# Kernel tuning notes

Measured on AMD Instinct MI355X. Metric: run time of the kernel, lower is better.

Reference implementation:

```python
import jax, jax.numpy as jnp
import numpy as np

EPS = 1e-8  # EPSILON in original repo (sharpen denom); cosine eps matches torch default 1e-8
MAX_SHIFT = 1
M_FEAT = 128


def _lstm_cell(x, h, c, W_ih, W_hh, b_ih, b_hh):
    gates = x @ W_ih.T + b_ih + h @ W_hh.T + b_hh
    i, f, g, o = jnp.split(gates, 4, axis=1)
    c_new = jax.nn.sigmoid(f) * c + jax.nn.sigmoid(i) * jnp.tanh(g)
    h_new = jax.nn.sigmoid(o) * jnp.tanh(c_new)
    return h_new, c_new


def _content_address(bank, k, b):
    # torch cosine_similarity over dim 2: dot / max(|m||k|, eps)
    dot = jnp.einsum('bnm,bm->bn', bank, k)
    denom = jnp.maximum(jnp.linalg.norm(bank, axis=2) * jnp.linalg.norm(k, axis=1, keepdims=True), 1e-8)
    return jax.nn.softmax(b * dot / denom, axis=1)


def _shift(w, s):
    # circular unroll then valid cross-correlation with per-batch kernel s [B, 2*MAX_SHIFT+1]
    wp = jnp.concatenate([w[:, -MAX_SHIFT:], w, w[:, :MAX_SHIFT]], axis=1)
    N = w.shape[1]
    taps = 2 * MAX_SHIFT + 1
    return sum(s[:, i:i + 1] * wp[:, i:i + N] for i in range(taps))


def _sharpen(w, r):
    wr = w ** r
    return wr / (wr.sum(axis=1, keepdims=True) + EPS)


def _move(bank, w_prev, k, b, g, s, r):
    w = _content_address(bank, k, b)
    w = w + (1.0 - g) * w_prev  # faithful: w_c is NOT scaled by g in the source
    w = _shift(w, s)
    return _sharpen(w, r)


def _split_read(p):
    M = M_FEAT
    k = p[:, :M]
    b = jax.nn.softplus(p[:, M:M + 1])
    g = jax.nn.sigmoid(p[:, M + 1:M + 2])
    s = jax.nn.softmax(p[:, M + 2:M + 5], axis=1)
    r = 1.0 + jax.nn.softplus(p[:, M + 5:M + 6])
    return k, b, g, s, r


def _split_write(p):
    M = M_FEAT
    k, b, g, s, r = _split_read(p[:, :M + 6])
    e = jax.nn.sigmoid(p[:, M + 6:M + 6 + M])
    a = p[:, M + 6 + M:M + 6 + 2 * M]
    return k, b, g, s, r, e, a


def setup_inputs() -> dict:
    key = jax.random.key(0)
    ks = jax.random.split(key, 16)
    B, E, H, N, M, O = 64, 256, 512, 4096, 128, 256
    rd_out, wr_out = M + 2 * MAX_SHIFT + 4, 3 * M + 2 * MAX_SHIFT + 4
    sc = 0.05
    return {
        'x': jax.random.normal(ks[0], (B, E), jnp.float32),
        'h_prev': jax.random.normal(ks[1], (B, H), jnp.float32),
        'c_prev': jax.random.normal(ks[2], (B, H), jnp.float32),
        'bank': jax.random.normal(ks[3], (B, N, M), jnp.float32) * 0.1,
        'read_w_prev': jnp.zeros((3, B, N), jnp.float32),
        'write_w_prev': jnp.zeros((3, B, N), jnp.float32),
        'W_ih': jax.random.normal(ks[4], (4 * H, E), jnp.float32) * sc,
        'W_hh': jax.random.normal(ks[5], (4 * H, H), jnp.float32) * sc,
        'b_ih': jax.random.normal(ks[6], (4 * H,), jnp.float32) * sc,
        'b_hh': jax.random.normal(ks[7], (4 * H,), jnp.float32) * sc,
        'read_W': jax.random.normal(ks[8], (3, rd_out, H), jnp.float32) * sc,
        'read_b': jax.random.normal(ks[9], (3, rd_out), jnp.float32) * sc,
        'write_W': jax.random.normal(ks[10], (3, wr_out, H), jnp.float32) * sc,
        'write_b': jax.random.normal(ks[11], (3, wr_out), jnp.float32) * sc,
        'out_W': jax.random.normal(ks[12], (O, 3 * M + H), jnp.float32) * sc,
        'out_b': jax.random.normal(ks[13], (O,), jnp.float32) * sc,
    }


def reference(x, h_prev, c_prev, bank, read_w_prev, write_w_prev,
              W_ih, W_hh, b_ih, b_hh, read_W, read_b, write_W, write_b,
              out_W, out_b):
    h, c = _lstm_cell(x, h_prev, c_prev, W_ih, W_hh, b_ih, b_hh)
    reads = []
    for i in range(3):  # head_num=3, structurally distinct params per head
        # write head: update bank
        pw = h @ write_W[i].T + write_b[i]
        k, b, g, s, r, e, a = _split_write(pw)
        ww = _move(bank, write_w_prev[i], k, b, g, s, r)
        bank = bank * (1.0 - ww[:, :, None] * e[:, None, :]) + ww[:, :, None] * a[:, None, :]
        # read head: read from updated bank
        pr = h @ read_W[i].T + read_b[i]
        k, b, g, s, r = _split_read(pr)
        wr = _move(bank, read_w_prev[i], k, b, g, s, r)
        reads.append(jnp.einsum('bn,bnm->bm', wr, bank))
    out = jnp.concatenate(reads + [h], axis=1) @ out_W.T + out_b
    return out
```

## Files before the change

kernel.cpp:

```cpp
#include <hip/hip_runtime.h>
#include <math.h>

namespace {

constexpr int kB = 64;
constexpr int kN = 4096;
constexpr int kM = 128;
constexpr int kH = 512;
constexpr int kE = 256;
constexpr int kO = 256;
constexpr int kGates = 4 * kH;
constexpr int kCatW = 3 * kM + kH;
constexpr int kPRow = 1600;
constexpr int kWN = kB * kN;

__device__ __forceinline__ float sigm_(float x) { return 1.f / (1.f + expf(-x)); }
__device__ __forceinline__ float softplus_(float x) { return x > 20.f ? x : log1pf(expf(x)); }

__global__ __launch_bounds__(256) void init_ws_k(float* gates, float* praw, float* cat,
                                                 float* out, const float* __restrict__ out_b) {
  int idx = blockIdx.x * 256 + threadIdx.x;
  if (idx < kB * kGates) gates[idx] = 0.f;
  if (idx < kB * kPRow)  praw[idx] = 0.f;
  if (idx < kB * 3 * kM) cat[(idx / 384) * kCatW + (idx % 384)] = 0.f;
  if (idx < kB * kO)     out[idx] = out_b[idx & (kO - 1)];
}

__global__ __launch_bounds__(256) void gemm_tn(const float* __restrict__ A, int lda,
                                               const float* __restrict__ W, int ldw,
                                               float* __restrict__ C, int ldc, int c0, int J) {
  __shared__ float As[64][68];
  __shared__ float Ws[64][68];
  const int tid = threadIdx.x;
  const int j0 = blockIdx.x * 64;
  const int b0 = (tid & 15) * 4;
  const int j4 = (tid >> 4) * 4;
  float acc[4][4] = {};
  for (int kc = 0; kc < 2; kc++) {
    const int k0 = blockIdx.y * 128 + kc * 64;
    __syncthreads();
#pragma unroll
    for (int i = 0; i < 4; i++) {
      int idx = tid + i * 256;
      int bb = idx >> 4;
      int kk = (idx & 15) * 4;
      float4 v = *(const float4*)(A + (size_t)bb * lda + k0 + kk);
      As[kk][bb] = v.x; As[kk + 1][bb] = v.y; As[kk + 2][bb] = v.z; As[kk + 3][bb] = v.w;
      float4 w = make_float4(0.f, 0.f, 0.f, 0.f);
      if (j0 + bb < J) w = *(const float4*)(W + (size_t)(j0 + bb) * ldw + k0 + kk);
      Ws[kk][bb] = w.x; Ws[kk + 1][bb] = w.y; Ws[kk + 2][bb] = w.z; Ws[kk + 3][bb] = w.w;
    }
    __syncthreads();
#pragma unroll 2
    for (int k = 0; k < 64; k++) {
      float4 av = *(const float4*)&As[k][b0];
      float4 wv = *(const float4*)&Ws[k][j4];
      float aa[4] = {av.x, av.y, av.z, av.w};
      float wwv[4] = {wv.x, wv.y, wv.z, wv.w};
#pragma unroll
      for (int ii = 0; ii < 4; ii++)
#pragma unroll
        for (int jj = 0; jj < 4; jj++) acc[ii][jj] += aa[ii] * wwv[jj];
    }
  }
#pragma unroll
  for (int ii = 0; ii < 4; ii++)
#pragma unroll
    for (int jj = 0; jj < 4; jj++) {
      int j = j0 + j4 + jj;
      if (j < J) atomicAdd(&C[(size_t)(b0 + ii) * ldc + c0 + j], acc[ii][jj]);
    }
}

__global__ __launch_bounds__(256) void lstm_nl(const float* __restrict__ gates,
                                               const float* __restrict__ b_ih,
                                               const float* __restrict__ b_hh,
                                               const float* __restrict__ c_prev,
                                               float* __restrict__ cat) {
  int idx = blockIdx.x * 256 + threadIdx.x;
  if (idx >= kB * kH) return;
  int b = idx >> 9;
  int hh = idx & (kH - 1);
  const float* g = gates + (size_t)b * kGates;
  float i_ = g[hh]            + b_ih[hh]            + b_hh[hh];
  float f_ = g[kH + hh]       + b_ih[kH + hh]       + b_hh[kH + hh];
  float g_ = g[2 * kH + hh]   + b_ih[2 * kH + hh]   + b_hh[2 * kH + hh];
  float o_ = g[3 * kH + hh]   + b_ih[3 * kH + hh]   + b_hh[3 * kH + hh];
  float c = sigm_(f_) * c_prev[idx] + sigm_(i_) * tanhf(g_);
  float h = sigm_(o_) * tanhf(c);
  cat[(size_t)b * kCatW + 3 * kM + hh] = h;
}

__global__ __launch_bounds__(128) void split_params(const float* __restrict__ praw,
                                                    const float* __restrict__ write_b,
                                                    const float* __restrict__ read_b,
                                                    float* __restrict__ kwb, float* __restrict__ krb,
                                                    float* __restrict__ evb, float* __restrict__ avb,
                                                    float* __restrict__ scal) {
  const int b = blockIdx.x;
  const int m = threadIdx.x;
  __shared__ float red[2];
  for (int i = 0; i < 3; i++) {
    const float* p = praw + (size_t)b * kPRow + i * 390;
    const float* wb = write_b + i * 390;
    float kv = p[m] + wb[m];
    kwb[((size_t)i * kB + b) * kM + m] = kv;
    evb[((size_t)i * kB + b) * kM + m] = sigm_(p[134 + m] + wb[134 + m]);
    avb[((size_t)i * kB + b) * kM + m] = p[262 + m] + wb[262 + m];
    float sq = kv * kv;
#pragma unroll
    for (int mm = 1; mm < 64; mm <<= 1) sq += __shfl_xor(sq, mm, 64);
    __syncthreads();
    if ((m & 63) == 0) red[m >> 6] = sq;
    __syncthreads();
    if (m == 0) {
      float* s = scal + ((size_t)i * kB + b) * 8;
      s[0] = softplus_(p[128] + wb[128]);
      s[1] = sigm_(p[129] + wb[129]);
      s[2] = 1.f + softplus_(p[133] + wb[133]);
      float x0 = p[130] + wb[130], x1 = p[131] + wb[131], x2 = p[132] + wb[132];
      float mx = fmaxf(x0, fmaxf(x1, x2));
      float e0 = expf(x0 - mx), e1 = expf(x1 - mx), e2 = expf(x2 - mx);
      float si = 1.f / (e0 + e1 + e2);
      s[3] = e0 * si; s[4] = e1 * si; s[5] = e2 * si;
      s[6] = sqrtf(red[0] + red[1]);
    }
  }
  for (int i = 0; i < 3; i++) {
    const float* p = praw + (size_t)b * kPRow + 1170 + i * 134;
    const float* rb = read_b + i * 134;
    float kv = p[m] + rb[m];
    krb[((size_t)i * kB + b) * kM + m] = kv;
    float sq = kv * kv;
#pragma unroll
    for (int mm = 1; mm < 64; mm <<= 1) sq += __shfl_xor(sq, mm, 64);
    __syncthreads();
    if ((m & 63) == 0) red[m >> 6] = sq;
    __syncthreads();
    if (m == 0) {
      float* s = scal + ((size_t)(3 + i) * kB + b) * 8;
      s[0] = softplus_(p[128] + rb[128]);
      s[1] = sigm_(p[129] + rb[129]);
      s[2] = 1.f + softplus_(p[133] + rb[133]);
      float x0 = p[130] + rb[130], x1 = p[131] + rb[131], x2 = p[132] + rb[132];
      float mx = fmaxf(x0, fmaxf(x1, x2));
      float e0 = expf(x0 - mx), e1 = expf(x1 - mx), e2 = expf(x2 - mx);
      float si = 1.f / (e0 + e1 + e2);
      s[3] = e0 * si; s[4] = e1 * si; s[5] = e2 * si;
      s[6] = sqrtf(red[0] + red[1]);
    }
  }
}

struct BankArgs {
  const float* bank;
  const float* cw[3];
  const float* ev[3];
  const float* av[3];
  const float* rw[3];
  float* ro[3];
  const float* k1;
  const float* k2;
  float* s1; float* s2; float* ssq;
};

template <int NC>
__global__ __launch_bounds__(256) void bank_pass(BankArgs A) {
  const int b = blockIdx.y;
  const int tid = threadIdx.x;
  const int lane = tid & 63;
  const int wv = tid >> 6;
  const int sub = lane >> 4;
  const int lm = lane & 15;
  const int m8 = lm * 8;
  constexpr int NCA = (NC > 0) ? NC : 1;
  float e_r[NCA][8], a_r[NCA][8];
#pragma unroll
  for (int j = 0; j < NC; j++)
#pragma unroll
    for (int t = 0; t < 8; t++) {
      e_r[j][t] = A.ev[j][b * kM + m8 + t];
      a_r[j][t] = A.av[j][b * kM + m8 + t];
    }
  const bool has1 = (A.s1 != nullptr);
  const bool has2 = (A.s2 != nullptr);
  float k1r[8] = {}, k2r[8] = {};
  if (has1) {
#pragma unroll
    for (int t = 0; t < 8; t++) k1r[t] = A.k1[b * kM + m8 + t];
  }
  if (has2) {
#pragma unroll
    for (int t = 0; t < 8; t++) k2r[t] = A.k2[b * kM + m8 + t];
  }
  float racc[3][8];
#pragma unroll
  for (int j = 0; j < 3; j++)
#pragma unroll
    for (int t = 0; t < 8; t++) racc[j][t] = 0.f;
  __shared__ float rlds[3][kM];
  if (tid < kM) { rlds[0][tid] = 0.f; rlds[1][tid] = 0.f; rlds[2][tid] = 0.f; }

  const size_t bbase = (size_t)b * kN * kM;
  const size_t brow = (size_t)b * kN;
  for (int it = 0; it < 16; it++) {
    const int row = blockIdx.x * 256 + it * 16 + wv * 4 + sub;
    const float* rp = A.bank + bbase + (size_t)row * kM + m8;
    float4 u0 = *(const float4*)rp;
    float4 u1 = *(const float4*)(rp + 4);
    float v[8] = {u0.x, u0.y, u0.z, u0.w, u1.x, u1.y, u1.z, u1.w};
#pragma unroll
    for (int j = 0; j < NC; j++) {
      const float wj = A.cw[j][brow + row];
#pragma unroll
      for (int t = 0; t < 8; t++) v[t] += wj * (a_r[j][t] - e_r[j][t] * v[t]);
      if (A.rw[j]) {
        const float rv = A.rw[j][brow + row];
#pragma unroll
        for (int t = 0; t < 8; t++) racc[j][t] += rv * v[t];
      }
    }
    if (has1) {
      float d1 = 0.f, d2 = 0.f, sq = 0.f;
#pragma unroll
      for (int t = 0; t < 8; t++) { d1 += v[t] * k1r[t]; sq += v[t] * v[t]; }
      if (has2) {
#pragma unroll
        for (int t = 0; t < 8; t++) d2 += v[t] * k2r[t];
      }
#pragma unroll
      for (int m = 1; m < 16; m <<= 1) {
        d1 += __shfl_xor(d1, m, 64);
        sq += __shfl_xor(sq, m, 64);
        if (has2) d2 += __shfl_xor(d2, m, 64);
      }
      if (lm == 0) {
        A.s1[brow + row] = d1;
        A.ssq[brow + row] = sq;
        if (has2) A.s2[brow + row] = d2;
      }
    }
  }
  if (A.rw[0] || A.rw[1] || A.rw[2]) {
    __syncthreads();
#pragma unroll
    for (int j = 0; j < 3; j++) {
      if (!A.rw[j]) continue;
#pragma unroll
      for (int t = 0; t < 8; t++) {
        racc[j][t] += __shfl_xor(racc[j][t], 16, 64);
        racc[j][t] += __shfl_xor(racc[j][t], 32, 64);
      }
      if (sub == 0) {
#pragma unroll
        for (int t = 0; t < 8; t++) atomicAdd(&rlds[j][m8 + t], racc[j][t]);
      }
    }
    __syncthreads();
    if (tid < kM) {
#pragma unroll
      for (int j = 0; j < 3; j++)
        if (A.rw[j]) atomicAdd(&A.ro[j][(size_t)b * kCatW + tid], rlds[j][tid]);
    }
  }
}

struct AddrArgs {
  const float* S[2];
  const float* R[2];
  const float* scal[2];
  const float* wprev[2];
  float* wout[2];
};

__global__ __launch_bounds__(256) void addressing(AddrArgs A) {
  const int b = blockIdx.x;
  const int hs = blockIdx.y;
  const float* S = A.S[hs] + (size_t)b * kN;
  const float* R = A.R[hs] + (size_t)b * kN;
  const float* sc = A.scal[hs] + b * 8;
  const float* wp = A.wprev[hs] + (size_t)b * kN;
  float* wo = A.wout[hs] + (size_t)b * kN;
  const float beta = sc[0], g = sc[1], r = sc[2];
  const float s0 = sc[3], s1 = sc[4], s2 = sc[5], kn = sc[6];
  __shared__ float wb[kN];
  __shared__ float red[4];
  const int tid = threadIdx.x;
  const int lane = tid & 63, wid = tid >> 6;
  float loc[16];
  float mx = -1e30f;
#pragma unroll
  for (int i = 0; i < 16; i++) {
    int n = tid + i * 256;
    float denom = fmaxf(sqrtf(R[n]) * kn, 1e-8f);
    float v = beta * S[n] / denom;
    loc[i] = v;
    mx = fmaxf(mx, v);
  }
#pragma unroll
  for (int m = 1; m < 64; m <<= 1) mx = fmaxf(mx, __shfl_xor(mx, m, 64));
  if (lane == 0) red[wid] = mx;
  __syncthreads();
  mx = fmaxf(fmaxf(red[0], red[1]), fmaxf(red[2], red[3]));
  float sum = 0.f;
#pragma unroll
  for (int i = 0; i < 16; i++) { loc[i] = expf(loc[i] - mx); sum += loc[i]; }
#pragma unroll
  for (int m = 1; m < 64; m <<= 1) sum += __shfl_xor(sum, m, 64);
  __syncthreads();
  if (lane == 0) red[wid] = sum;
  __syncthreads();
  sum = red[0] + red[1] + red[2] + red[3];
  const float inv = 1.f / sum;
  const float omg = 1.f - g;
#pragma unroll
  for (int i = 0; i < 16; i++) {
    int n = tid + i * 256;
    wb[n] = loc[i] * inv + omg * wp[n];
  }
  __syncthreads();
  float ssum = 0.f;
#pragma unroll
  for (int i = 0; i < 16; i++) {
    int n = tid + i * 256;
    float sh = s0 * wb[(n + kN - 1) & (kN - 1)] + s1 * wb[n] + s2 * wb[(n + 1) & (kN - 1)];
    float y = powf(sh, r);
    loc[i] = y;
    ssum += y;
  }
#pragma unroll
  for (int m = 1; m < 64; m <<= 1) ssum += __shfl_xor(ssum, m, 64);
  __syncthreads();
  if (lane == 0) red[wid] = ssum;
  __syncthreads();
  ssum = red[0] + red[1] + red[2] + red[3];
  const float invs = 1.f / (ssum + 1e-8f);
#pragma unroll
  for (int i = 0; i < 16; i++) {
    int n = tid + i * 256;
    wo[n] = loc[i] * invs;
  }
}

}

extern "C" void kernel_launch(void* const* d_in, const int* in_sizes, int n_in,
                              void* d_out, int out_size, void* d_ws, size_t ws_size,
                              hipStream_t stream) {
  const float* x            = (const float*)d_in[0];
  const float* h_prev       = (const float*)d_in[1];
  const float* c_prev       = (const float*)d_in[2];
  const float* bank         = (const float*)d_in[3];
  const float* read_w_prev  = (const float*)d_in[4];
  const float* write_w_prev = (const float*)d_in[5];
  const float* W_ih         = (const float*)d_in[6];
  const float* W_hh         = (const float*)d_in[7];
  const float* b_ih         = (const float*)d_in[8];
  const float* b_hh         = (const float*)d_in[9];
  const float* read_W       = (const float*)d_in[10];
  const float* read_b       = (const float*)d_in[11];
  const float* write_W      = (const float*)d_in[12];
  const float* write_b      = (const float*)d_in[13];
  const float* out_W        = (const float*)d_in[14];
  const float* out_b        = (const float*)d_in[15];
  float* out = (float*)d_out;

  float* ws    = (float*)d_ws;
  float* gates = ws;
  float* praw  = gates + kB * kGates;
  float* cat   = praw + kB * kPRow;
  float* kwb   = cat + kB * kCatW;
  float* krb   = kwb + 3 * kB * kM;
  float* evb   = krb + 3 * kB * kM;
  float* avb   = evb + 3 * kB * kM;
  float* scal  = avb + 3 * kB * kM;
  float* S1    = scal + 6 * kB * 8;
  float* S2    = S1 + kWN;
  float* SSq   = S2 + kWN;
  float* wwv   = SSq + kWN;
  float* wrv   = wwv + 3 * kWN;

  init_ws_k<<<512, 256, 0, stream>>>(gates, praw, cat, out, out_b);
  gemm_tn<<<dim3(kGates / 64, kE / 128), 256, 0, stream>>>(x, kE, W_ih, kE, gates, kGates, 0, kGates);
  gemm_tn<<<dim3(kGates / 64, kH / 128), 256, 0, stream>>>(h_prev, kH, W_hh, kH, gates, kGates, 0, kGates);
  lstm_nl<<<(kB * kH) / 256, 256, 0, stream>>>(gates, b_ih, b_hh, c_prev, cat);
  gemm_tn<<<dim3(19, kH / 128), 256, 0, stream>>>(cat + 3 * kM, kCatW, write_W, kH, praw, kPRow, 0, 1170);
  gemm_tn<<<dim3(7, kH / 128), 256, 0, stream>>>(cat + 3 * kM, kCatW, read_W, kH, praw, kPRow, 1170, 402);
  split_params<<<64, 128, 0, stream>>>(praw, write_b, read_b, kwb, krb, evb, avb, scal);

  {
    BankArgs p = {};
    p.bank = bank;
    p.k1 = kwb; p.s1 = S1; p.s2 = nullptr; p.ssq = SSq;
    bank_pass<0><<<dim3(16, kB), 256, 0, stream>>>(p);
  }
  {
    AddrArgs a = {};
    a.S[0] = S1; a.R[0] = SSq; a.scal[0] = scal + 0;
    a.wprev[0] = write_w_prev; a.wout[0] = wwv;
    a.S[1] = a.S[0]; a.R[1] = a.R[0]; a.scal[1] = a.scal[0]; a.wprev[1] = a.wprev[0]; a.wout[1] = a.wout[0];
    addressing<<<dim3(64, 1), 256, 0, stream>>>(a);
  }
  {
    BankArgs p = {};
    p.bank = bank;
    p.cw[0] = wwv; p.ev[0] = evb; p.av[0] = avb;
    p.k1 = krb; p.k2 = kwb + kB * kM;
    p.s1 = S1; p.s2 = S2; p.ssq = SSq;
    bank_pass<1><<<dim3(16, kB), 256, 0, stream>>>(p);
  }
  {
    AddrArgs a = {};
    a.S[0] = S1; a.R[0] = SSq; a.scal[0] = scal + (size_t)3 * kB * 8;
    a.wprev[0] = read_w_prev; a.wout[0] = wrv;
    a.S[1] = S2; a.R[1] = SSq; a.scal[1] = scal + (size_t)1 * kB * 8;
    a.wprev[1] = write_w_prev + kWN; a.wout[1] = wwv + kWN;
    addressing<<<dim3(64, 2), 256, 0, stream>>>(a);
  }
  {
    BankArgs p = {};
    p.bank = bank;
    p.cw[0] = wwv;        p.ev[0] = evb;            p.av[0] = avb;
    p.cw[1] = wwv + kWN;  p.ev[1] = evb + kB * kM;  p.av[1] = avb + kB * kM;
    p.rw[0] = wrv; p.ro[0] = cat;
    p.k1 = krb + kB * kM; p.k2 = kwb + 2 * kB * kM;
    p.s1 = S1; p.s2 = S2; p.ssq = SSq;
    bank_pass<2><<<dim3(16, kB), 256, 0, stream>>>(p);
  }
  {
    AddrArgs a = {};
    a.S[0] = S1; a.R[0] = SSq; a.scal[0] = scal + (size_t)4 * kB * 8;
    a.wprev[0] = read_w_prev + kWN; a.wout[0] = wrv + kWN;
    a.S[1] = S2; a.R[1] = SSq; a.scal[1] = scal + (size_t)2 * kB * 8;
    a.wprev[1] = write_w_prev + 2 * kWN; a.wout[1] = wwv + 2 * kWN;
    addressing<<<dim3(64, 2), 256, 0, stream>>>(a);
  }
  {
    BankArgs p = {};
    p.bank = bank;
    p.cw[0] = wwv;           p.ev[0] = evb;                p.av[0] = avb;
    p.cw[1] = wwv + kWN;     p.ev[1] = evb + kB * kM;      p.av[1] = avb + kB * kM;
    p.cw[2] = wwv + 2 * kWN; p.ev[2] = evb + 2 * kB * kM;  p.av[2] = avb + 2 * kB * kM;
    p.k1 = krb + 2 * kB * kM;
    p.s1 = S1; p.s2 = nullptr; p.ssq = SSq;
    bank_pass<3><<<dim3(16, kB), 256, 0, stream>>>(p);
  }
  {
    AddrArgs a = {};
    a.S[0] = S1; a.R[0] = SSq; a.scal[0] = scal + (size_t)5 * kB * 8;
    a.wprev[0] = read_w_prev + 2 * kWN; a.wout[0] = wrv + 2 * kWN;
    a.S[1] = a.S[0]; a.R[1] = a.R[0]; a.scal[1] = a.scal[0]; a.wprev[1] = a.wprev[0]; a.wout[1] = a.wout[0];
    addressing<<<dim3(64, 1), 256, 0, stream>>>(a);
  }
  {
    BankArgs p = {};
    p.bank = bank;
    p.cw[0] = wwv;           p.ev[0] = evb;                p.av[0] = avb;
    p.cw[1] = wwv + kWN;     p.ev[1] = evb + kB * kM;      p.av[1] = avb + kB * kM;
    p.cw[2] = wwv + 2 * kWN; p.ev[2] = evb + 2 * kB * kM;  p.av[2] = avb + 2 * kB * kM;
    p.rw[1] = wrv + kWN;     p.ro[1] = cat + kM;
    p.rw[2] = wrv + 2 * kWN; p.ro[2] = cat + 2 * kM;
    p.s1 = nullptr; p.s2 = nullptr; p.ssq = nullptr;
    bank_pass<3><<<dim3(16, kB), 256, 0, stream>>>(p);
  }
  gemm_tn<<<dim3(kO / 64, kCatW / 128), 256, 0, stream>>>(cat, kCatW, out_W, kCatW, out, kO, 0, kO);

  (void)in_sizes; (void)n_in; (void)out_size; (void)ws_size;
}
```

Baseline: 494.0 us.

## Fuse addressing into bank passes via last-block counters and merge GEMM launches

The separate addressing kernels are folded into the tail of each bank_pass. An atomic per-batch counter lets the last of the 16 blocks for a batch compute the softmax, shift and sharpen weights. The small GEMMs are merged: the x and h gate GEMMs become one non-split-K kernel that writes directly and also does the workspace init, and the write and read projections become one kernel. This removes launches, atomics and zero-init passes. The cost is that the gate and projection GEMMs now run on very few blocks (33 and 25) with the full K loop each, and each pass now uses distinct scratch buffers.

```diff
diff --git a/kernel.cpp b/kernel.cpp
--- a/kernel.cpp
+++ b/kernel.cpp
@@ -17,18 +17,22 @@
 __device__ __forceinline__ float sigm_(float x) { return 1.f / (1.f + expf(-x)); }
 __device__ __forceinline__ float softplus_(float x) { return x > 20.f ? x : log1pf(expf(x)); }
 
-__global__ __launch_bounds__(256) void init_ws_k(float* gates, float* praw, float* cat,
-                                                 float* out, const float* __restrict__ out_b) {
-  int idx = blockIdx.x * 256 + threadIdx.x;
-  if (idx < kB * kGates) gates[idx] = 0.f;
-  if (idx < kB * kPRow)  praw[idx] = 0.f;
-  if (idx < kB * 3 * kM) cat[(idx / 384) * kCatW + (idx % 384)] = 0.f;
-  if (idx < kB * kO)     out[idx] = out_b[idx & (kO - 1)];
-}
-
-__global__ __launch_bounds__(256) void gemm_tn(const float* __restrict__ A, int lda,
-                                               const float* __restrict__ W, int ldw,
-                                               float* __restrict__ C, int ldc, int c0, int J) {
+__global__ __launch_bounds__(256) void gates_gemm(const float* __restrict__ x,
+                                                  const float* __restrict__ W_ih,
+                                                  const float* __restrict__ h_prev,
+                                                  const float* __restrict__ W_hh,
+                                                  float* __restrict__ gates,
+                                                  const float* __restrict__ out_b,
+                                                  float* __restrict__ out,
+                                                  float* __restrict__ cat,
+                                                  int* __restrict__ cnt) {
+  if (blockIdx.x == 32) {
+    const int tid = threadIdx.x;
+    for (int i = tid; i < kB * kO; i += 256) out[i] = out_b[i & (kO - 1)];
+    for (int i = tid; i < kB * 384; i += 256) cat[(i / 384) * kCatW + (i % 384)] = 0.f;
+    for (int i = tid; i < 512; i += 256) cnt[i] = 0;
+    return;
+  }
   __shared__ float As[64][68];
   __shared__ float Ws[64][68];
   const int tid = threadIdx.x;
@@ -36,8 +40,12 @@
   const int b0 = (tid & 15) * 4;
   const int j4 = (tid >> 4) * 4;
   float acc[4][4] = {};
-  for (int kc = 0; kc < 2; kc++) {
-    const int k0 = blockIdx.y * 128 + kc * 64;
+  for (int kc = 0; kc < 12; kc++) {
+    const bool isx = kc < 4;
+    const float* A = isx ? x : h_prev;
+    const float* W = isx ? W_ih : W_hh;
+    const int lda = isx ? kE : kH;
+    const int k0 = (isx ? kc : (kc - 4)) * 64;
     __syncthreads();
 #pragma unroll
     for (int i = 0; i < 4; i++) {
@@ -46,8 +54,7 @@
       int kk = (idx & 15) * 4;
       float4 v = *(const float4*)(A + (size_t)bb * lda + k0 + kk);
       As[kk][bb] = v.x; As[kk + 1][bb] = v.y; As[kk + 2][bb] = v.z; As[kk + 3][bb] = v.w;
-      float4 w = make_float4(0.f, 0.f, 0.f, 0.f);
-      if (j0 + bb < J) w = *(const float4*)(W + (size_t)(j0 + bb) * ldw + k0 + kk);
+      float4 w = *(const float4*)(W + (size_t)(j0 + bb) * lda + k0 + kk);
       Ws[kk][bb] = w.x; Ws[kk + 1][bb] = w.y; Ws[kk + 2][bb] = w.z; Ws[kk + 3][bb] = w.w;
     }
     __syncthreads();
@@ -56,20 +63,18 @@
       float4 av = *(const float4*)&As[k][b0];
       float4 wv = *(const float4*)&Ws[k][j4];
       float aa[4] = {av.x, av.y, av.z, av.w};
-      float wwv[4] = {wv.x, wv.y, wv.z, wv.w};
+      float ww[4] = {wv.x, wv.y, wv.z, wv.w};
 #pragma unroll
       for (int ii = 0; ii < 4; ii++)
 #pragma unroll
-        for (int jj = 0; jj < 4; jj++) acc[ii][jj] += aa[ii] * wwv[jj];
-    }
-  }
-#pragma unroll
-  for (int ii = 0; ii < 4; ii++)
-#pragma unroll
-    for (int jj = 0; jj < 4; jj++) {
-      int j = j0 + j4 + jj;
-      if (j < J) atomicAdd(&C[(size_t)(b0 + ii) * ldc + c0 + j], acc[ii][jj]);
-    }
+        for (int jj = 0; jj < 4; jj++) acc[ii][jj] += aa[ii] * ww[jj];
+    }
+  }
+#pragma unroll
+  for (int ii = 0; ii < 4; ii++) {
+    float4 st = make_float4(acc[ii][0], acc[ii][1], acc[ii][2], acc[ii][3]);
+    *(float4*)&gates[(size_t)(b0 + ii) * kGates + j0 + j4] = st;
+  }
 }
 
 __global__ __launch_bounds__(256) void lstm_nl(const float* __restrict__ gates,
@@ -82,13 +87,63 @@
   int b = idx >> 9;
   int hh = idx & (kH - 1);
   const float* g = gates + (size_t)b * kGates;
-  float i_ = g[hh]            + b_ih[hh]            + b_hh[hh];
-  float f_ = g[kH + hh]       + b_ih[kH + hh]       + b_hh[kH + hh];
-  float g_ = g[2 * kH + hh]   + b_ih[2 * kH + hh]   + b_hh[2 * kH + hh];
-  float o_ = g[3 * kH + hh]   + b_ih[3 * kH + hh]   + b_hh[3 * kH + hh];
+  float i_ = g[hh]          + b_ih[hh]          + b_hh[hh];
+  float f_ = g[kH + hh]     + b_ih[kH + hh]     + b_hh[kH + hh];
+  float g_ = g[2 * kH + hh] + b_ih[2 * kH + hh] + b_hh[2 * kH + hh];
+  float o_ = g[3 * kH + hh] + b_ih[3 * kH + hh] + b_hh[3 * kH + hh];
   float c = sigm_(f_) * c_prev[idx] + sigm_(i_) * tanhf(g_);
   float h = sigm_(o_) * tanhf(c);
   cat[(size_t)b * kCatW + 3 * kM + hh] = h;
+}
+
+__global__ __launch_bounds__(256) void proj_gemm(const float* __restrict__ cat,
+                                                 const float* __restrict__ write_W,
+                                                 const float* __restrict__ read_W,
+                                                 float* __restrict__ praw) {
+  __shared__ float As[64][68];
+  __shared__ float Ws[64][68];
+  const float* A = cat + 3 * kM;
+  const int tid = threadIdx.x;
+  const int j0 = blockIdx.x * 64;
+  const int b0 = (tid & 15) * 4;
+  const int j4 = (tid >> 4) * 4;
+  float acc[4][4] = {};
+  for (int kc = 0; kc < 8; kc++) {
+    const int k0 = kc * 64;
+    __syncthreads();
+#pragma unroll
+    for (int i = 0; i < 4; i++) {
+      int idx = tid + i * 256;
+      int bb = idx >> 4;
+      int kk = (idx & 15) * 4;
+      float4 v = *(const float4*)(A + (size_t)bb * kCatW + k0 + kk);
+      As[kk][bb] = v.x; As[kk + 1][bb] = v.y; As[kk + 2][bb] = v.z; As[kk + 3][bb] = v.w;
+      int j = j0 + bb;
+      float4 w = make_float4(0.f, 0.f, 0.f, 0.f);
+      if (j < 1170)       w = *(const float4*)(write_W + (size_t)j * kH + k0 + kk);
+      else if (j < 1572)  w = *(const float4*)(read_W + (size_t)(j - 1170) * kH + k0 + kk);
+      Ws[kk][bb] = w.x; Ws[kk + 1][bb] = w.y; Ws[kk + 2][bb] = w.z; Ws[kk + 3][bb] = w.w;
+    }
+    __syncthreads();
+#pragma unroll 2
+    for (int k = 0; k < 64; k++) {
+      float4 av = *(const float4*)&As[k][b0];
+      float4 wv = *(const float4*)&Ws[k][j4];
+      float aa[4] = {av.x, av.y, av.z, av.w};
+      float ww[4] = {wv.x, wv.y, wv.z, wv.w};
+#pragma unroll
+      for (int ii = 0; ii < 4; ii++)
+#pragma unroll
+        for (int jj = 0; jj < 4; jj++) acc[ii][jj] += aa[ii] * ww[jj];
+    }
+  }
+  if (j0 + j4 < 1572) {
+#pragma unroll
+    for (int ii = 0; ii < 4; ii++) {
+      float4 st = make_float4(acc[ii][0], acc[ii][1], acc[ii][2], acc[ii][3]);
+      *(float4*)&praw[(size_t)(b0 + ii) * kPRow + j0 + j4] = st;
+    }
+  }
 }
 
 __global__ __launch_bounds__(128) void split_params(const float* __restrict__ praw,
@@ -152,6 +207,69 @@
   }
 }
 
+__device__ void addr_tail(const float* __restrict__ S, const float* __restrict__ R,
+                          const float* __restrict__ sc, const float* __restrict__ wp,
+                          float* __restrict__ wo, float* wb, float* red, int tid) {
+  const float beta = sc[0], g = sc[1], r = sc[2];
+  const float s0 = sc[3], s1 = sc[4], s2 = sc[5], kn = sc[6];
+  const int lane = tid & 63, wid = tid >> 6;
+  float loc[16];
+  float mx = -1e30f;
+#pragma unroll
+  for (int i = 0; i < 16; i++) {
+    int n = tid + i * 256;
+    float denom = fmaxf(sqrtf(R[n]) * kn, 1e-8f);
+    float v = beta * S[n] / denom;
+    loc[i] = v;
+    mx = fmaxf(mx, v);
+  }
+#pragma unroll
+  for (int m = 1; m < 64; m <<= 1) mx = fmaxf(mx, __shfl_xor(mx, m, 64));
+  __syncthreads();
+  if (lane == 0) red[wid] = mx;
+  __syncthreads();
+  mx = fmaxf(fmaxf(red[0], red[1]), fmaxf(red[2], red[3]));
+  float sum = 0.f;
+#pragma unroll
+  for (int i = 0; i < 16; i++) { loc[i] = expf(loc[i] - mx); sum += loc[i]; }
+#pragma unroll
+  for (int m = 1; m < 64; m <<= 1) sum += __shfl_xor(sum, m, 64);
+  __syncthreads();
+  if (lane == 0) red[wid] = sum;
+  __syncthreads();
+  sum = red[0] + red[1] + red[2] + red[3];
+  const float inv = 1.f / sum;
+  const float omg = 1.f - g;
+#pragma unroll
+  for (int i = 0; i < 16; i++) {
+    int n = tid + i * 256;
+    wb[n] = loc[i] * inv + omg * wp[n];
+  }
+  __syncthreads();
+  float ssum = 0.f;
+#pragma unroll
+  for (int i = 0; i < 16; i++) {
+    int n = tid + i * 256;
+    float sh = s0 * wb[(n + kN - 1) & (kN - 1)] + s1 * wb[n] + s2 * wb[(n + 1) & (kN - 1)];
+    float y = powf(sh, r);
+    loc[i] = y;
+    ssum += y;
+  }
+#pragma unroll
+  for (int m = 1; m < 64; m <<= 1) ssum += __shfl_xor(ssum, m, 64);
+  __syncthreads();
+  if (lane == 0) red[wid] = ssum;
+  __syncthreads();
+  ssum = red[0] + red[1] + red[2] + red[3];
+  const float invs = 1.f / (ssum + 1e-8f);
+#pragma unroll
+  for (int i = 0; i < 16; i++) {
+    int n = tid + i * 256;
+    wo[n] = loc[i] * invs;
+  }
+  __syncthreads();
+}
+
 struct BankArgs {
   const float* bank;
   const float* cw[3];
@@ -162,9 +280,12 @@
   const float* k1;
   const float* k2;
   float* s1; float* s2; float* ssq;
+  const float* scal0; const float* wp0; float* wo0;
+  const float* scal1; const float* wp1; float* wo1;
+  int* cnt;
 };
 
-template <int NC>
+template <int NC, int NH>
 __global__ __launch_bounds__(256) void bank_pass(BankArgs A) {
   const int b = blockIdx.y;
   const int tid = threadIdx.x;
@@ -182,14 +303,12 @@
       e_r[j][t] = A.ev[j][b * kM + m8 + t];
       a_r[j][t] = A.av[j][b * kM + m8 + t];
     }
-  const bool has1 = (A.s1 != nullptr);
-  const bool has2 = (A.s2 != nullptr);
   float k1r[8] = {}, k2r[8] = {};
-  if (has1) {
+  if (NH >= 1) {
 #pragma unroll
     for (int t = 0; t < 8; t++) k1r[t] = A.k1[b * kM + m8 + t];
   }
-  if (has2) {
+  if (NH >= 2) {
 #pragma unroll
     for (int t = 0; t < 8; t++) k2r[t] = A.k2[b * kM + m8 + t];
   }
@@ -199,10 +318,14 @@
 #pragma unroll
     for (int t = 0; t < 8; t++) racc[j][t] = 0.f;
   __shared__ float rlds[3][kM];
+  __shared__ float wb_s[kN];
+  __shared__ float red_s[4];
+  __shared__ int job_s;
   if (tid < kM) { rlds[0][tid] = 0.f; rlds[1][tid] = 0.f; rlds[2][tid] = 0.f; }
 
   const size_t bbase = (size_t)b * kN * kM;
   const size_t brow = (size_t)b * kN;
+#pragma unroll 2
   for (int it = 0; it < 16; it++) {
     const int row = blockIdx.x * 256 + it * 16 + wv * 4 + sub;
     const float* rp = A.bank + bbase + (size_t)row * kM + m8;
@@ -220,11 +343,11 @@
         for (int t = 0; t < 8; t++) racc[j][t] += rv * v[t];
       }
     }
-    if (has1) {
+    if (NH >= 1) {
       float d1 = 0.f, d2 = 0.f, sq = 0.f;
 #pragma unroll
       for (int t = 0; t < 8; t++) { d1 += v[t] * k1r[t]; sq += v[t] * v[t]; }
-      if (has2) {
+      if (NH >= 2) {
 #pragma unroll
         for (int t = 0; t < 8; t++) d2 += v[t] * k2r[t];
       }
@@ -232,12 +355,12 @@
       for (int m = 1; m < 16; m <<= 1) {
         d1 += __shfl_xor(d1, m, 64);
         sq += __shfl_xor(sq, m, 64);
-        if (has2) d2 += __shfl_xor(d2, m, 64);
+        if (NH >= 2) d2 += __shfl_xor(d2, m, 64);
       }
       if (lm == 0) {
         A.s1[brow + row] = d1;
         A.ssq[brow + row] = sq;
-        if (has2) A.s2[brow + row] = d2;
+        if (NH >= 2) A.s2[brow + row] = d2;
       }
     }
   }
@@ -263,83 +386,70 @@
         if (A.rw[j]) atomicAdd(&A.ro[j][(size_t)b * kCatW + tid], rlds[j][tid]);
     }
   }
-}
-
-struct AddrArgs {
-  const float* S[2];
-  const float* R[2];
-  const float* scal[2];
-  const float* wprev[2];
-  float* wout[2];
-};
-
-__global__ __launch_bounds__(256) void addressing(AddrArgs A) {
-  const int b = blockIdx.x;
-  const int hs = blockIdx.y;
-  const float* S = A.S[hs] + (size_t)b * kN;
-  const float* R = A.R[hs] + (size_t)b * kN;
-  const float* sc = A.scal[hs] + b * 8;
-  const float* wp = A.wprev[hs] + (size_t)b * kN;
-  float* wo = A.wout[hs] + (size_t)b * kN;
-  const float beta = sc[0], g = sc[1], r = sc[2];
-  const float s0 = sc[3], s1 = sc[4], s2 = sc[5], kn = sc[6];
-  __shared__ float wb[kN];
-  __shared__ float red[4];
+  if (NH > 0) {
+    __syncthreads();
+    if (tid == 0) {
+      __threadfence();
+      int j = 0;
+      if (atomicAdd(&A.cnt[b * 2 + 0], 1) == 15) j |= 1;
+      if (NH > 1 && atomicAdd(&A.cnt[b * 2 + 1], 1) == 15) j |= 2;
+      job_s = j;
+    }
+    __syncthreads();
+    const int job = job_s;
+    if (job) {
+      __threadfence();
+      if (job & 1)
+        addr_tail(A.s1 + brow, A.ssq + brow, A.scal0 + b * 8, A.wp0 + brow, A.wo0 + brow,
+                  wb_s, red_s, tid);
+      if (job & 2)
+        addr_tail(A.s2 + brow, A.ssq + brow, A.scal1 + b * 8, A.wp1 + brow, A.wo1 + brow,
+                  wb_s, red_s, tid);
+    }
+  }
+}
+
+__global__ __launch_bounds__(256) void out_gemm(const float* __restrict__ A,
+                                                const float* __restrict__ W,
+                                                float* __restrict__ C) {
+  __shared__ float As[64][68];
+  __shared__ float Ws[64][68];
   const int tid = threadIdx.x;
-  const int lane = tid & 63, wid = tid >> 6;
-  float loc[16];
-  float mx = -1e30f;
-#pragma unroll
-  for (int i = 0; i < 16; i++) {
-    int n = tid + i * 256;
-    float denom = fmaxf(sqrtf(R[n]) * kn, 1e-8f);
-    float v = beta * S[n] / denom;
-    loc[i] = v;
-    mx = fmaxf(mx, v);
-  }
-#pragma unroll
-  for (int m = 1; m < 64; m <<= 1) mx = fmaxf(mx, __shfl_xor(mx, m, 64));
-  if (lane == 0) red[wid] = mx;
-  __syncthreads();
-  mx = fmaxf(fmaxf(red[0], red[1]), fmaxf(red[2], red[3]));
-  float sum = 0.f;
-#pragma unroll
-  for (int i = 0; i < 16; i++) { loc[i] = expf(loc[i] - mx); sum += loc[i]; }
-#pragma unroll
-  for (int m = 1; m < 64; m <<= 1) sum += __shfl_xor(sum, m, 64);
-  __syncthreads();
-  if (lane == 0) red[wid] = sum;
-  __syncthreads();
-  sum = red[0] + red[1] + red[2] + red[3];
-  const float inv = 1.f / sum;
-  const float omg = 1.f - g;
-#pragma unroll
-  for (int i = 0; i < 16; i++) {
-    int n = tid + i * 256;
-    wb[n] = loc[i] * inv + omg * wp[n];
-  }
-  __syncthreads();
-  float ssum = 0.f;
-#pragma unroll
-  for (int i = 0; i < 16; i++) {
-    int n = tid + i * 256;
-    float sh = s0 * wb[(n + kN - 1) & (kN - 1)] + s1 * wb[n] + s2 * wb[(n + 1) & (kN - 1)];
-    float y = powf(sh, r);
-    loc[i] = y;
-    ssum += y;
-  }
-#pragma unroll
-  for (int m = 1; m < 64; m <<= 1) ssum += __shfl_xor(ssum, m, 64);
-  __syncthreads();
-  if (lane == 0) red[wid] = ssum;
-  __syncthreads();
-  ssum = red[0] + red[1] + red[2] + red[3];
-  const float invs = 1.f / (ssum + 1e-8f);
-#pragma unroll
-  for (int i = 0; i < 16; i++) {
-    int n = tid + i * 256;
-    wo[n] = loc[i] * invs;
-  }
+  const int j0 = blockIdx.x * 64;
+  const int b0 = (tid & 15) * 4;
+  const int j4 = (tid >> 4) * 4;
+  float acc[4][4] = {};
+  for (int kc = 0; kc < 2; kc++) {
+    const int k0 = blockIdx.y * 128 + kc * 64;
+    __syncthreads();
+#pragma unroll
+    for (int i = 0; i < 4; i++) {
+      int idx = tid + i * 256;
+      int bb = idx >> 4;
+      int kk = (idx & 15) * 4;
+      float4 v = *(const float4*)(A + (size_t)bb * kCatW + k0 + kk);
+      As[kk][bb] = v.x; As[kk + 1][bb] = v.y; As[kk + 2][bb] = v.z; As[kk + 3][bb] = v.w;
+      float4 w = *(const float4*)(W + (size_t)(j0 + bb) * kCatW + k0 + kk);
+      Ws[kk][bb] = w.x; Ws[kk + 1][bb] = w.y; Ws[kk + 2][bb] = w.z; Ws[kk + 3][bb] = w.w;
+    }
+    __syncthreads();
+#pragma unroll 2
+    for (int k = 0; k < 64; k++) {
+      float4 av = *(const float4*)&As[k][b0];
+      float4 wv = *(const float4*)&Ws[k][j4];
+      float aa[4] = {av.x, av.y, av.z, av.w};
+      float ww[4] = {wv.x, wv.y, wv.z, wv.w};
+#pragma unroll
+      for (int ii = 0; ii < 4; ii++)
+#pragma unroll
+        for (int jj = 0; jj < 4; jj++) acc[ii][jj] += aa[ii] * ww[jj];
+    }
+  }
+#pragma unroll
+  for (int ii = 0; ii < 4; ii++)
+#pragma unroll
+    for (int jj = 0; jj < 4; jj++)
+      atomicAdd(&C[(size_t)(b0 + ii) * kO + j0 + j4 + jj], acc[ii][jj]);
 }
 
 }
@@ -374,48 +484,39 @@
   float* evb   = krb + 3 * kB * kM;
   float* avb   = evb + 3 * kB * kM;
   float* scal  = avb + 3 * kB * kM;
-  float* S1    = scal + 6 * kB * 8;
-  float* S2    = S1 + kWN;
-  float* SSq   = S2 + kWN;
-  float* wwv   = SSq + kWN;
+  float* wwv   = scal + 6 * kB * 8;
   float* wrv   = wwv + 3 * kWN;
-
-  init_ws_k<<<512, 256, 0, stream>>>(gates, praw, cat, out, out_b);
-  gemm_tn<<<dim3(kGates / 64, kE / 128), 256, 0, stream>>>(x, kE, W_ih, kE, gates, kGates, 0, kGates);
-  gemm_tn<<<dim3(kGates / 64, kH / 128), 256, 0, stream>>>(h_prev, kH, W_hh, kH, gates, kGates, 0, kGates);
+  float* sc_p  = wrv + 3 * kWN;
+  float* S_p1  = sc_p + 0 * kWN;  float* Q_p1 = sc_p + 1 * kWN;
+  float* Sa_p2 = sc_p + 2 * kWN;  float* Sb_p2 = sc_p + 3 * kWN;  float* Q_p2 = sc_p + 4 * kWN;
+  float* Sa_p3 = sc_p + 5 * kWN;  float* Sb_p3 = sc_p + 6 * kWN;  float* Q_p3 = sc_p + 7 * kWN;
+  float* S_p4  = sc_p + 8 * kWN;  float* Q_p4 = sc_p + 9 * kWN;
+  int* cnt = (int*)(sc_p + 10 * kWN);
+
+  gates_gemm<<<33, 256, 0, stream>>>(x, W_ih, h_prev, W_hh, gates, out_b, out, cat, cnt);
   lstm_nl<<<(kB * kH) / 256, 256, 0, stream>>>(gates, b_ih, b_hh, c_prev, cat);
-  gemm_tn<<<dim3(19, kH / 128), 256, 0, stream>>>(cat + 3 * kM, kCatW, write_W, kH, praw, kPRow, 0, 1170);
-  gemm_tn<<<dim3(7, kH / 128), 256, 0, stream>>>(cat + 3 * kM, kCatW, read_W, kH, praw, kPRow, 1170, 402);
+  proj_gemm<<<25, 256, 0, stream>>>(cat, write_W, read_W, praw);
   split_params<<<64, 128, 0, stream>>>(praw, write_b, read_b, kwb, krb, evb, avb, scal);
 
   {
     BankArgs p = {};
     p.bank = bank;
-    p.k1 = kwb; p.s1 = S1; p.s2 = nullptr; p.ssq = SSq;
-    bank_pass<0><<<dim3(16, kB), 256, 0, stream>>>(p);
-  }
-  {
-    AddrArgs a = {};
-    a.S[0] = S1; a.R[0] = SSq; a.scal[0] = scal + 0;
-    a.wprev[0] = write_w_prev; a.wout[0] = wwv;
-    a.S[1] = a.S[0]; a.R[1] = a.R[0]; a.scal[1] = a.scal[0]; a.wprev[1] = a.wprev[0]; a.wout[1] = a.wout[0];
-    addressing<<<dim3(64, 1), 256, 0, stream>>>(a);
+    p.k1 = kwb; p.s1 = S_p1; p.ssq = Q_p1;
+    p.scal0 = scal + 0; p.wp0 = write_w_prev; p.wo0 = wwv;
+    p.cnt = cnt + 0 * 128;
+    bank_pass<0, 1><<<dim3(16, kB), 256, 0, stream>>>(p);
   }
   {
     BankArgs p = {};
     p.bank = bank;
     p.cw[0] = wwv; p.ev[0] = evb; p.av[0] = avb;
-    p.k1 = krb; p.k2 = kwb + kB * kM;
-    p.s1 = S1; p.s2 = S2; p.ssq = SSq;
-    bank_pass<1><<<dim3(16, kB), 256, 0, stream>>>(p);
-  }
-  {
-    AddrArgs a = {};
-    a.S[0] = S1; a.R[0] = SSq; a.scal[0] = scal + (size_t)3 * kB * 8;
-    a.wprev[0] = read_w_prev; a.wout[0] = wrv;
-    a.S[1] = S2; a.R[1] = SSq; a.scal[1] = scal + (size_t)1 * kB * 8;
-    a.wprev[1] = write_w_prev + kWN; a.wout[1] = wwv + kWN;
-    addressing<<<dim3(64, 2), 256, 0, stream>>>(a);
+    p.k1 = krb;             p.s1 = Sa_p2;
+    p.k2 = kwb + kB * kM;   p.s2 = Sb_p2;
+    p.ssq = Q_p2;
+    p.scal0 = scal + (size_t)3 * kB * 8; p.wp0 = read_w_prev;        p.wo0 = wrv;
+    p.scal1 = scal + (size_t)1 * kB * 8; p.wp1 = write_w_prev + kWN; p.wo1 = wwv + kWN;
+    p.cnt = cnt + 1 * 128;
+    bank_pass<1, 2><<<dim3(16, kB), 256, 0, stream>>>(p);
   }
   {
     BankArgs p = {};
@@ -423,17 +524,13 @@
     p.cw[0] = wwv;        p.ev[0] = evb;            p.av[0] = avb;
     p.cw[1] = wwv + kWN;  p.ev[1] = evb + kB * kM;  p.av[1] = avb + kB * kM;
     p.rw[0] = wrv; p.ro[0] = cat;
-    p.k1 = krb + kB * kM; p.k2 = kwb + 2 * kB * kM;
-    p.s1 = S1; p.s2 = S2; p.ssq = SSq;
-    bank_pass<2><<<dim3(16, kB), 256, 0, stream>>>(p);
-  }
-  {
-    AddrArgs a = {};
-    a.S[0] = S1; a.R[0] = SSq; a.scal[0] = scal + (size_t)4 * kB * 8;
-    a.wprev[0] = read_w_prev + kWN; a.wout[0] = wrv + kWN;
-    a.S[1] = S2; a.R[1] = SSq; a.scal[1] = scal + (size_t)2 * kB * 8;
-    a.wprev[1] = write_w_prev + 2 * kWN; a.wout[1] = wwv + 2 * kWN;
-    addressing<<<dim3(64, 2), 256, 0, stream>>>(a);
+    p.k1 = krb + kB * kM;     p.s1 = Sa_p3;
+    p.k2 = kwb + 2 * kB * kM; p.s2 = Sb_p3;
+    p.ssq = Q_p3;
+    p.scal0 = scal + (size_t)4 * kB * 8; p.wp0 = read_w_prev + kWN;      p.wo0 = wrv + kWN;
+    p.scal1 = scal + (size_t)2 * kB * 8; p.wp1 = write_w_prev + 2 * kWN; p.wo1 = wwv + 2 * kWN;
+    p.cnt = cnt + 2 * 128;
+    bank_pass<2, 2><<<dim3(16, kB), 256, 0, stream>>>(p);
   }
   {
     BankArgs p = {};
@@ -441,16 +538,10 @@
     p.cw[0] = wwv;           p.ev[0] = evb;                p.av[0] = avb;
     p.cw[1] = wwv + kWN;     p.ev[1] = evb + kB * kM;      p.av[1] = avb + kB * kM;
     p.cw[2] = wwv + 2 * kWN; p.ev[2] = evb + 2 * kB * kM;  p.av[2] = avb + 2 * kB * kM;
-    p.k1 = krb + 2 * kB * kM;
-    p.s1 = S1; p.s2 = nullptr; p.ssq = SSq;
-    bank_pass<3><<<dim3(16, kB), 256, 0, stream>>>(p);
-  }
-  {
-    AddrArgs a = {};
-    a.S[0] = S1; a.R[0] = SSq; a.scal[0] = scal + (size_t)5 * kB * 8;
-    a.wprev[0] = read_w_prev + 2 * kWN; a.wout[0] = wrv + 2 * kWN;
-    a.S[1] = a.S[0]; a.R[1] = a.R[0]; a.scal[1] = a.scal[0]; a.wprev[1] = a.wprev[0]; a.wout[1] = a.wout[0];
-    addressing<<<dim3(64, 1), 256, 0, stream>>>(a);
+    p.k1 = krb + 2 * kB * kM; p.s1 = S_p4; p.ssq = Q_p4;
+    p.scal0 = scal + (size_t)5 * kB * 8; p.wp0 = read_w_prev + 2 * kWN; p.wo0 = wrv + 2 * kWN;
+    p.cnt = cnt + 3 * 128;
+    bank_pass<3, 1><<<dim3(16, kB), 256, 0, stream>>>(p);
   }
   {
     BankArgs p = {};
@@ -460,10 +551,9 @@
     p.cw[2] = wwv + 2 * kWN; p.ev[2] = evb + 2 * kB * kM;  p.av[2] = avb + 2 * kB * kM;
     p.rw[1] = wrv + kWN;     p.ro[1] = cat + kM;
     p.rw[2] = wrv + 2 * kWN; p.ro[2] = cat + 2 * kM;
-    p.s1 = nullptr; p.s2 = nullptr; p.ssq = nullptr;
-    bank_pass<3><<<dim3(16, kB), 256, 0, stream>>>(p);
-  }
-  gemm_tn<<<dim3(kO / 64, kCatW / 128), 256, 0, stream>>>(cat, kCatW, out_W, kCatW, out, kO, 0, kO);
+    bank_pass<3, 0><<<dim3(16, kB), 256, 0, stream>>>(p);
+  }
+  out_gemm<<<dim3(kO / 64, kCatW / 128), 256, 0, stream>>>(cat, out_W, out);
 
   (void)in_sizes; (void)n_in; (void)out_size; (void)ws_size;
 }
```

New measurement: 799.7 us. 1.62x slower.
